# Performance work log

Measured on AMD Instinct MI355X. Metric: run time of the kernel, lower is better.

Reference implementation:

```python
import jax, jax.numpy as jnp
import numpy as np

TOP_K = 2

def setup_inputs() -> dict:
    key = jax.random.key(0)
    k1, k2, k3, k4 = jax.random.split(key, 4)
    T, H, I, E = 8192, 2048, 4096, 8
    s = 0.02
    return {
        "hidden_states": jax.random.normal(k1, (T, H), dtype=jnp.float32),
        "router_w": jax.random.normal(k2, (E, H), dtype=jnp.float32) * s,
        "ws": jax.random.normal(k3, (E, 2 * I, H), dtype=jnp.float32) * s,  # [gate; up]
        "w2s": jax.random.normal(k4, (E, H, I), dtype=jnp.float32) * s,
    }

def reference(hidden_states, router_w, ws, w2s):
    # Router gating: softmax over experts, top-k, NO renormalization
    logits = hidden_states @ router_w.T              # [T, E]
    probs = jax.nn.softmax(logits, axis=-1)
    topv, topi = jax.lax.top_k(probs, TOP_K)         # [T, K]
    T, E = probs.shape
    I = w2s.shape[2]
    # Dense routing-weight matrix [T, E]; top_k indices are unique per token
    w = jnp.zeros_like(probs).at[jnp.arange(T)[:, None], topi].set(topv)
    out = jnp.zeros_like(hidden_states)
    for e in range(E):  # fixed small expert loop; avoids [T,E,2I] blowup
        gate = hidden_states @ ws[e, :I].T           # [T, I]
        up = hidden_states @ ws[e, I:].T             # [T, I]
        h = jax.nn.silu(gate) * up                   # SwiGLU
        out = out + w[:, e:e + 1] * (h @ w2s[e].T)   # combine
    return out
```

## Files before the change

### kernel.cpp

```cpp
#include <hip/hip_runtime.h>
#include <cstdint>
#include <cstddef>

#define T_TOK 8192
#define HDIM  2048
#define IDIM  4096
#define NEXP  8
#define MAXT  72

typedef __bf16 bf16x8 __attribute__((ext_vector_type(8)));
typedef float  f32x4  __attribute__((ext_vector_type(4)));

#define BARRIER() __builtin_amdgcn_s_barrier()
#define VMW(n)    do { asm volatile("s_waitcnt vmcnt(" #n ")" ::: "memory"); } while (0)
#define PRIO1()   __builtin_amdgcn_s_setprio(1)
#define PRIO0()   __builtin_amdgcn_s_setprio(0)

__device__ __forceinline__ unsigned short f2bf(float f) {
    union { float f; unsigned u; } v; v.f = f;
    unsigned r = v.u + 0x7FFFu + ((v.u >> 16) & 1u);
    return (unsigned short)(r >> 16);
}

__device__ __forceinline__ void gload16(const void* g, void* l) {
    __builtin_amdgcn_global_load_lds((__attribute__((address_space(1))) void*)g,
                                     (__attribute__((address_space(3))) void*)l,
                                     16, 0, 0);
}

__global__ __launch_bounds__(256) void router_k(const float* __restrict__ hs,
                                                const float* __restrict__ rw,
                                                float* __restrict__ wgt,
                                                int* __restrict__ counts,
                                                int* __restrict__ lists,
                                                unsigned short* __restrict__ hs_bf) {
    int gid  = blockIdx.x * 256 + threadIdx.x;
    int tok  = gid >> 6;
    int lane = threadIdx.x & 63;
    const float* x = hs + (size_t)tok * HDIM;
    unsigned short* xb = hs_bf + (size_t)tok * HDIM;

    float acc[NEXP];
#pragma unroll
    for (int e = 0; e < NEXP; ++e) acc[e] = 0.f;
    for (int h = lane; h < HDIM; h += 64) {
        float xv = x[h];
        xb[h] = f2bf(xv);
#pragma unroll
        for (int e = 0; e < NEXP; ++e) acc[e] = fmaf(xv, rw[e * HDIM + h], acc[e]);
    }
#pragma unroll
    for (int off = 32; off > 0; off >>= 1) {
#pragma unroll
        for (int e = 0; e < NEXP; ++e) acc[e] += __shfl_xor(acc[e], off, 64);
    }
    if (lane == 0) {
        float m = acc[0];
#pragma unroll
        for (int e = 1; e < NEXP; ++e) m = fmaxf(m, acc[e]);
        float p[NEXP]; float s = 0.f;
#pragma unroll
        for (int e = 0; e < NEXP; ++e) { p[e] = expf(acc[e] - m); s += p[e]; }
        float inv = 1.f / s;
        int i1 = 0;
#pragma unroll
        for (int e = 1; e < NEXP; ++e) if (acc[e] > acc[i1]) i1 = e;
        int i2 = -1;
#pragma unroll
        for (int e = 0; e < NEXP; ++e) if (e != i1 && (i2 < 0 || acc[e] > acc[i2])) i2 = e;
#pragma unroll
        for (int e = 0; e < NEXP; ++e)
            wgt[(size_t)tok * NEXP + e] = (e == i1 || e == i2) ? p[e] * inv : 0.f;
        int p1 = atomicAdd(&counts[i1], 1);
        lists[i1 * T_TOK + p1] = tok;
        int p2 = atomicAdd(&counts[i2], 1);
        lists[i2 * T_TOK + p2] = (1 << 16) | tok;
    }
}

__global__ void plan_k(const int* __restrict__ counts, int* __restrict__ offs,
                       int* __restrict__ desc, int* __restrict__ ntiles) {
    if (threadIdx.x == 0 && blockIdx.x == 0) {
        int off = 0, n = 0;
        for (int e = 0; e < NEXP; ++e) {
            offs[e] = off;
            int nt = (counts[e] + 255) >> 8;
            for (int t = 0; t < nt; ++t) desc[n++] = (e << 16) | t;
            off += nt * 256;
        }
        *ntiles = n;
    }
}

__global__ __launch_bounds__(256) void cvt_k(const float* __restrict__ in,
                                             unsigned short* __restrict__ out, long n4) {
    long i      = (long)blockIdx.x * 256 + threadIdx.x;
    long stride = (long)gridDim.x * 256;
    const float4* in4 = (const float4*)in;
    ushort4* out4 = (ushort4*)out;
    for (long j = i; j < n4; j += stride) {
        float4 v = in4[j];
        ushort4 o;
        o.x = f2bf(v.x); o.y = f2bf(v.y); o.z = f2bf(v.z); o.w = f2bf(v.w);
        out4[j] = o;
    }
}

__global__ __launch_bounds__(512, 2) void gemm1_k(const unsigned short* __restrict__ A,
                                                  const unsigned short* __restrict__ Wall,
                                                  unsigned short* __restrict__ Hout,
                                                  const int* __restrict__ lists,
                                                  const int* __restrict__ counts,
                                                  const int* __restrict__ offs,
                                                  const int* __restrict__ desc,
                                                  const int* __restrict__ ntiles) {
    const int slot = blockIdx.y;
    if (slot >= *ntiles) return;
    const int dsc = desc[slot];
    const int e = dsc >> 16, tt = dsc & 0xFFFF;
    const int cnt = counts[e];
    const int t0 = tt * 256;
    const int* list = lists + e * T_TOK;
    const unsigned short* W = Wall + (size_t)e * 2 * IDIM * HDIM;
    const int hbase = offs[e];
    const int n0 = blockIdx.x * 128;

    extern __shared__ __align__(16) char lds[];

    const int tid  = threadIdx.x;
    const int lane = tid & 63;
    const int wid  = tid >> 6;
    const int wr   = wid >> 2;
    const int wc   = wid & 3;

    const int prow = tid >> 3;
    const int pcol = (tid & 7) * 16;
    const int lcol = (pcol ^ ((prow & 7) << 4)) >> 1;
    unsigned aoff[4];
#pragma unroll
    for (int i = 0; i < 4; ++i) {
        int g = t0 + i * 64 + prow;
        int tok = list[(g < cnt) ? g : t0] & 0xFFFF;
        aoff[i] = (unsigned)tok * HDIM + lcol;
    }
    unsigned goff[2], uoff[2];
#pragma unroll
    for (int i = 0; i < 2; ++i) {
        goff[i] = (unsigned)(n0 + i * 64 + prow) * HDIM + lcol;
        uoff[i] = (unsigned)(IDIM + n0 + i * 64 + prow) * HDIM + lcol;
    }
    const int dst = tid * 16;

#define SG_AH0(b, t) do { unsigned k0_ = (unsigned)((t) & 31) * 64;      \
    gload16(A + aoff[0] + k0_, lds + (b) * 32768 + dst);                 \
    gload16(A + aoff[1] + k0_, lds + (b) * 32768 + 8192 + dst); } while (0)
#define SG_AH1(b, t) do { unsigned k0_ = (unsigned)((t) & 31) * 64;      \
    gload16(A + aoff[2] + k0_, lds + (b) * 32768 + 16384 + dst);         \
    gload16(A + aoff[3] + k0_, lds + (b) * 32768 + 24576 + dst); } while (0)
#define SG_G(b, t) do { unsigned k0_ = (unsigned)((t) & 31) * 64;        \
    gload16(W + goff[0] + k0_, lds + 65536 + (b) * 16384 + dst);         \
    gload16(W + goff[1] + k0_, lds + 65536 + (b) * 16384 + 8192 + dst); } while (0)
#define SG_U(b, t) do { unsigned k0_ = (unsigned)((t) & 31) * 64;        \
    gload16(W + uoff[0] + k0_, lds + 98304 + (b) * 16384 + dst);         \
    gload16(W + uoff[1] + k0_, lds + 98304 + (b) * 16384 + 8192 + dst); } while (0)

    const int frd = (lane & 7) << 4;
    const int cb0 = (((lane >> 4) * 16)     ) ^ frd;
    const int cb1 = (((lane >> 4) * 16) | 64) ^ frd;
    const int arow = (wr * 64 + (lane & 15)) * 128;
    const int brow = (wc * 32 + (lane & 15)) * 128;

    f32x4 accg[8][2], accu[8][2];
#pragma unroll
    for (int mi = 0; mi < 8; ++mi)
#pragma unroll
        for (int ni = 0; ni < 2; ++ni) {
            accg[mi][ni] = (f32x4){0.f, 0.f, 0.f, 0.f};
            accu[mi][ni] = (f32x4){0.f, 0.f, 0.f, 0.f};
        }

    SG_AH0(0, 0); SG_G(0, 0); SG_U(0, 0); SG_AH1(0, 0);
    SG_AH0(1, 1); SG_G(1, 1);
    VMW(4);
    BARRIER();

    const int NT = HDIM / 64;
    for (int kt = 0; kt < NT; ++kt) {
        const int b  = kt & 1;
        const int bn = b ^ 1;
        const char* la = lds + b * 32768 + arow;
        const char* lg = lds + 65536 + b * 16384 + brow;
        const char* lu = lds + 98304 + b * 16384 + brow;
        bf16x8 a0[2][4], bg[2][2], bu[2][2];

#pragma unroll
        for (int mi = 0; mi < 4; ++mi) {
            a0[0][mi] = *(const bf16x8*)(la + mi * 2048 + cb0);
            a0[1][mi] = *(const bf16x8*)(la + mi * 2048 + cb1);
        }
#pragma unroll
        for (int ni = 0; ni < 2; ++ni) {
            bg[0][ni] = *(const bf16x8*)(lg + ni * 2048 + cb0);
            bg[1][ni] = *(const bf16x8*)(lg + ni * 2048 + cb1);
        }
        SG_AH1(bn, kt + 1);
        BARRIER(); PRIO1();
#pragma unroll
        for (int ks = 0; ks < 2; ++ks)
#pragma unroll
            for (int mi = 0; mi < 4; ++mi)
#pragma unroll
                for (int ni = 0; ni < 2; ++ni)
                    accg[mi][ni] = __builtin_amdgcn_mfma_f32_16x16x32_bf16(a0[ks][mi], bg[ks][ni], accg[mi][ni], 0, 0, 0);
        PRIO0(); BARRIER();

#pragma unroll
        for (int ni = 0; ni < 2; ++ni) {
            bu[0][ni] = *(const bf16x8*)(lu + ni * 2048 + cb0);
            bu[1][ni] = *(const bf16x8*)(lu + ni * 2048 + cb1);
        }
        SG_U(bn, kt + 1);
        BARRIER(); PRIO1();
#pragma unroll
        for (int ks = 0; ks < 2; ++ks)
#pragma unroll
            for (int mi = 0; mi < 4; ++mi)
#pragma unroll
                for (int ni = 0; ni < 2; ++ni)
                    accu[mi][ni] = __builtin_amdgcn_mfma_f32_16x16x32_bf16(a0[ks][mi], bu[ks][ni], accu[mi][ni], 0, 0, 0);
        PRIO0(); BARRIER();

#pragma unroll
        for (int mi = 0; mi < 4; ++mi) {
            a0[0][mi] = *(const bf16x8*)(la + 16384 + mi * 2048 + cb0);
            a0[1][mi] = *(const bf16x8*)(la + 16384 + mi * 2048 + cb1);
        }
        SG_AH0(b, kt + 2);
        BARRIER(); PRIO1();
#pragma unroll
        for (int ks = 0; ks < 2; ++ks)
#pragma unroll
            for (int mi = 0; mi < 4; ++mi)
#pragma unroll
                for (int ni = 0; ni < 2; ++ni)
                    accg[mi + 4][ni] = __builtin_amdgcn_mfma_f32_16x16x32_bf16(a0[ks][mi], bg[ks][ni], accg[mi + 4][ni], 0, 0, 0);
        PRIO0(); BARRIER();

        SG_G(b, kt + 2);
        PRIO1();
#pragma unroll
        for (int ks = 0; ks < 2; ++ks)
#pragma unroll
            for (int mi = 0; mi < 4; ++mi)
#pragma unroll
                for (int ni = 0; ni < 2; ++ni)
                    accu[mi + 4][ni] = __builtin_amdgcn_mfma_f32_16x16x32_bf16(a0[ks][mi], bu[ks][ni], accu[mi + 4][ni], 0, 0, 0);
        PRIO0();
        VMW(4);
        BARRIER();
    }
    VMW(0);
#undef SG_AH0
#undef SG_AH1
#undef SG_G
#undef SG_U

#pragma unroll
    for (int mi = 0; mi < 8; ++mi)
#pragma unroll
        for (int ni = 0; ni < 2; ++ni)
#pragma unroll
            for (int j = 0; j < 4; ++j) {
                int qr = mi >> 2, m = mi & 3;
                int row = hbase + t0 + qr * 128 + wr * 64 + m * 16 + ((lane >> 4) << 2) + j;
                int col = n0 + wc * 32 + ni * 16 + (lane & 15);
                float g = accg[mi][ni][j], u = accu[mi][ni][j];
                float hv = (g / (1.f + expf(-g))) * u;
                Hout[(size_t)row * IDIM + col] = f2bf(hv);
            }
}

__global__ __launch_bounds__(512, 2) void gemm2_k(const unsigned short* __restrict__ Ah,
                                                  const unsigned short* __restrict__ Ball,
                                                  const float* __restrict__ wgt,
                                                  float* __restrict__ outP,
                                                  const int* __restrict__ lists,
                                                  const int* __restrict__ counts,
                                                  const int* __restrict__ offs,
                                                  const int* __restrict__ desc,
                                                  const int* __restrict__ ntiles) {
    const int slot = blockIdx.y;
    if (slot >= *ntiles) return;
    const int dsc = desc[slot];
    const int e = dsc >> 16, tt = dsc & 0xFFFF;
    const int cnt = counts[e];
    const int t0 = tt * 256;
    const int* list = lists + e * T_TOK;
    const unsigned short* B = Ball + (size_t)e * HDIM * IDIM;
    const int hbase = offs[e];
    const int n0 = blockIdx.x * 256;

    extern __shared__ __align__(16) char lds[];

    const int tid  = threadIdx.x;
    const int lane = tid & 63;
    const int wid  = tid >> 6;
    const int wr   = wid >> 2;
    const int wc   = wid & 3;

    const int prow = tid >> 3;
    const int pcol = (tid & 7) * 16;
    const int lcol = (pcol ^ ((prow & 7) << 4)) >> 1;
    unsigned aoff[4], boff[4];
#pragma unroll
    for (int i = 0; i < 4; ++i) {
        aoff[i] = (unsigned)(hbase + t0 + i * 64 + prow) * IDIM + lcol;
        boff[i] = (unsigned)(n0 + i * 64 + prow) * IDIM + lcol;
    }
    const int dst = tid * 16;

#define SG_AH0(b, t) do { unsigned k0_ = (unsigned)((t) & 63) * 64;       \
    gload16(Ah + aoff[0] + k0_, lds + (b) * 32768 + dst);                 \
    gload16(Ah + aoff[1] + k0_, lds + (b) * 32768 + 8192 + dst); } while (0)
#define SG_AH1(b, t) do { unsigned k0_ = (unsigned)((t) & 63) * 64;       \
    gload16(Ah + aoff[2] + k0_, lds + (b) * 32768 + 16384 + dst);         \
    gload16(Ah + aoff[3] + k0_, lds + (b) * 32768 + 24576 + dst); } while (0)
#define SG_BH0(b, t) do { unsigned k0_ = (unsigned)((t) & 63) * 64;       \
    gload16(B + boff[0] + k0_, lds + 65536 + (b) * 32768 + dst);          \
    gload16(B + boff[1] + k0_, lds + 65536 + (b) * 32768 + 8192 + dst); } while (0)
#define SG_BH1(b, t) do { unsigned k0_ = (unsigned)((t) & 63) * 64;       \
    gload16(B + boff[2] + k0_, lds + 65536 + (b) * 32768 + 16384 + dst);  \
    gload16(B + boff[3] + k0_, lds + 65536 + (b) * 32768 + 24576 + dst); } while (0)

    const int frd = (lane & 7) << 4;
    const int cb0 = (((lane >> 4) * 16)     ) ^ frd;
    const int cb1 = (((lane >> 4) * 16) | 64) ^ frd;
    const int arow = (wr * 64 + (lane & 15)) * 128;
    const int brow = (wc * 64 + (lane & 15)) * 128;

    f32x4 acc[8][4];
#pragma unroll
    for (int mi = 0; mi < 8; ++mi)
#pragma unroll
        for (int ni = 0; ni < 4; ++ni) acc[mi][ni] = (f32x4){0.f, 0.f, 0.f, 0.f};

    SG_AH0(0, 0); SG_BH0(0, 0); SG_AH1(0, 0); SG_BH1(0, 0);
    SG_AH0(1, 1); SG_BH0(1, 1);
    VMW(0);
    BARRIER();

    const int NT = IDIM / 64;
    for (int kt = 0; kt < NT; ++kt) {
        const int b  = kt & 1;
        const int bn = b ^ 1;
        const char* la = lds + b * 32768 + arow;
        const char* lb = lds + 65536 + b * 32768 + brow;
        bf16x8 a0[2][4], bb[2][4];

#pragma unroll
        for (int mi = 0; mi < 4; ++mi) {
            a0[0][mi] = *(const bf16x8*)(la + mi * 2048 + cb0);
            a0[1][mi] = *(const bf16x8*)(la + mi * 2048 + cb1);
        }
#pragma unroll
        for (int ni = 0; ni < 2; ++ni) {
            bb[0][ni] = *(const bf16x8*)(lb + ni * 2048 + cb0);
            bb[1][ni] = *(const bf16x8*)(lb + ni * 2048 + cb1);
        }
        SG_AH1(bn, kt + 1);
        BARRIER(); PRIO1();
#pragma unroll
        for (int ks = 0; ks < 2; ++ks)
#pragma unroll
            for (int mi = 0; mi < 4; ++mi)
#pragma unroll
                for (int ni = 0; ni < 2; ++ni)
                    acc[mi][ni] = __builtin_amdgcn_mfma_f32_16x16x32_bf16(a0[ks][mi], bb[ks][ni], acc[mi][ni], 0, 0, 0);
        PRIO0(); BARRIER();

#pragma unroll
        for (int ni = 0; ni < 2; ++ni) {
            bb[0][ni + 2] = *(const bf16x8*)(lb + (ni + 2) * 2048 + cb0);
            bb[1][ni + 2] = *(const bf16x8*)(lb + (ni + 2) * 2048 + cb1);
        }
        SG_BH1(bn, kt + 1);
        BARRIER(); PRIO1();
#pragma unroll
        for (int ks = 0; ks < 2; ++ks)
#pragma unroll
            for (int mi = 0; mi < 4; ++mi)
#pragma unroll
                for (int ni = 0; ni < 2; ++ni)
                    acc[mi][ni + 2] = __builtin_amdgcn_mfma_f32_16x16x32_bf16(a0[ks][mi], bb[ks][ni + 2], acc[mi][ni + 2], 0, 0, 0);
        PRIO0(); BARRIER();

#pragma unroll
        for (int mi = 0; mi < 4; ++mi) {
            a0[0][mi] = *(const bf16x8*)(la + 16384 + mi * 2048 + cb0);
            a0[1][mi] = *(const bf16x8*)(la + 16384 + mi * 2048 + cb1);
        }
        SG_AH0(b, kt + 2);
        BARRIER(); PRIO1();
#pragma unroll
        for (int ks = 0; ks < 2; ++ks)
#pragma unroll
            for (int mi = 0; mi < 4; ++mi)
#pragma unroll
                for (int ni = 0; ni < 2; ++ni)
                    acc[mi + 4][ni] = __builtin_amdgcn_mfma_f32_16x16x32_bf16(a0[ks][mi], bb[ks][ni], acc[mi + 4][ni], 0, 0, 0);
        PRIO0(); BARRIER();

        SG_BH0(b, kt + 2);
        PRIO1();
#pragma unroll
        for (int ks = 0; ks < 2; ++ks)
#pragma unroll
            for (int mi = 0; mi < 4; ++mi)
#pragma unroll
                for (int ni = 0; ni < 2; ++ni)
                    acc[mi + 4][ni + 2] = __builtin_amdgcn_mfma_f32_16x16x32_bf16(a0[ks][mi], bb[ks][ni + 2], acc[mi + 4][ni + 2], 0, 0, 0);
        PRIO0();
        VMW(4);
        BARRIER();
    }
    VMW(0);
#undef SG_AH0
#undef SG_AH1
#undef SG_BH0
#undef SG_BH1

#pragma unroll
    for (int mi = 0; mi < 8; ++mi) {
        int qr = mi >> 2, m = mi & 3;
#pragma unroll
        for (int j = 0; j < 4; ++j) {
            int g = t0 + qr * 128 + wr * 64 + m * 16 + ((lane >> 4) << 2) + j;
            if (g < cnt) {
                int ent = list[g];
                int tok = ent & 0xFFFF;
                int sl  = ent >> 16;
                float w = wgt[(size_t)tok * NEXP + e];
                float* o = outP + (size_t)sl * T_TOK * HDIM + (size_t)tok * HDIM;
#pragma unroll
                for (int ni = 0; ni < 4; ++ni) {
                    int col = n0 + wc * 64 + ni * 16 + (lane & 15);
                    o[col] = w * acc[mi][ni][j];
                }
            }
        }
    }
}

__global__ __launch_bounds__(256) void combine_k(const float* __restrict__ p0,
                                                 const float* __restrict__ p1,
                                                 float* __restrict__ out, long n4) {
    long i      = (long)blockIdx.x * 256 + threadIdx.x;
    long stride = (long)gridDim.x * 256;
    const float4* a4 = (const float4*)p0;
    const float4* b4 = (const float4*)p1;
    float4* o4 = (float4*)out;
    for (long j = i; j < n4; j += stride) {
        float4 a = a4[j], b = b4[j];
        o4[j] = make_float4(a.x + b.x, a.y + b.y, a.z + b.z, a.w + b.w);
    }
}

extern "C" void kernel_launch(void* const* d_in, const int* in_sizes, int n_in,
                              void* d_out, int out_size, void* d_ws, size_t ws_size,
                              hipStream_t stream) {
    const float* hs  = (const float*)d_in[0];
    const float* rw  = (const float*)d_in[1];
    const float* ws  = (const float*)d_in[2];
    const float* w2s = (const float*)d_in[3];
    float* out = (float*)d_out;

    char* wsp = (char*)d_ws;
    unsigned short* hs_bf = (unsigned short*)(wsp);
    unsigned short* w_bf  = (unsigned short*)(wsp + 33554432ULL);
    unsigned short* w2_bf = (unsigned short*)(wsp + 301989888ULL);
    unsigned short* h_bf  = (unsigned short*)(wsp + 436207616ULL);
    float*          outP  = (float*)(wsp + 587202560ULL);
    float*          wgt   = (float*)(wsp + 721420288ULL);
    int*            counts = (int*)(wsp + 721682432ULL);
    int*            offs   = (int*)(wsp + 721682560ULL);
    int*            lists  = (int*)(wsp + 721682688ULL);
    int*            desc   = (int*)(wsp + 721944832ULL);
    int*            ntiles = (int*)(wsp + 721945344ULL);

    hipMemsetAsync(counts, 0, NEXP * sizeof(int), stream);
    cvt_k<<<4096, 256, 0, stream>>>(ws, w_bf, (long)NEXP * 2 * IDIM * HDIM / 4);
    cvt_k<<<4096, 256, 0, stream>>>(w2s, w2_bf, (long)NEXP * HDIM * IDIM / 4);
    router_k<<<(T_TOK * 64) / 256, 256, 0, stream>>>(hs, rw, wgt, counts, lists, hs_bf);
    plan_k<<<1, 64, 0, stream>>>(counts, offs, desc, ntiles);

    gemm1_k<<<dim3(IDIM / 128, MAXT), 512, 131072, stream>>>(
        hs_bf, w_bf, h_bf, lists, counts, offs, desc, ntiles);
    gemm2_k<<<dim3(HDIM / 256, MAXT), 512, 131072, stream>>>(
        h_bf, w2_bf, wgt, outP, lists, counts, offs, desc, ntiles);
    combine_k<<<2048, 256, 0, stream>>>(outP, outP + (size_t)T_TOK * HDIM, out,
                                        (long)T_TOK * HDIM / 4);
}
```

Baseline: 1.368 ms.

## Software-pipeline LDS fragment reads across iterations and drop redundant barriers

Both MoE GEMM kernels now load the next k-tile's A and B fragments from LDS at the end of the current iteration, so each phase's LDS reads overlap the MFMAs of the phase before. Separate a1 and b23 register sets let fragment loads run ahead of the matching compute. This removes several barriers per iteration and moves the vmcnt wait ahead of the prefetch reads. The down-projection prologue now waits with vmcnt(4) instead of 0. The cost is higher register pressure and a tighter ordering argument between LDS reads and async global-to-LDS writes into the other buffer.

```diff
diff --git a/kernel.cpp b/kernel.cpp
--- a/kernel.cpp
+++ b/kernel.cpp
@@ -184,27 +184,38 @@
     VMW(4);
     BARRIER();
 
+    bf16x8 a0[2][4], a1[2][4], bg[2][2], bu[2][2];
+    {
+        const char* la = lds + arow;
+        const char* lg = lds + 65536 + brow;
+#pragma unroll
+        for (int mi = 0; mi < 4; ++mi) {
+            a0[0][mi] = *(const bf16x8*)(la + mi * 2048 + cb0);
+            a0[1][mi] = *(const bf16x8*)(la + mi * 2048 + cb1);
+        }
+#pragma unroll
+        for (int ni = 0; ni < 2; ++ni) {
+            bg[0][ni] = *(const bf16x8*)(lg + ni * 2048 + cb0);
+            bg[1][ni] = *(const bf16x8*)(lg + ni * 2048 + cb1);
+        }
+    }
+
     const int NT = HDIM / 64;
     for (int kt = 0; kt < NT; ++kt) {
         const int b  = kt & 1;
         const int bn = b ^ 1;
-        const char* la = lds + b * 32768 + arow;
-        const char* lg = lds + 65536 + b * 16384 + brow;
-        const char* lu = lds + 98304 + b * 16384 + brow;
-        bf16x8 a0[2][4], bg[2][2], bu[2][2];
-
-#pragma unroll
-        for (int mi = 0; mi < 4; ++mi) {
-            a0[0][mi] = *(const bf16x8*)(la + mi * 2048 + cb0);
-            a0[1][mi] = *(const bf16x8*)(la + mi * 2048 + cb1);
-        }
-#pragma unroll
-        for (int ni = 0; ni < 2; ++ni) {
-            bg[0][ni] = *(const bf16x8*)(lg + ni * 2048 + cb0);
-            bg[1][ni] = *(const bf16x8*)(lg + ni * 2048 + cb1);
+        const char* la  = lds + b * 32768 + arow;
+        const char* lu  = lds + 98304 + b * 16384 + brow;
+        const char* lan = lds + bn * 32768 + arow;
+        const char* lgn = lds + 65536 + bn * 16384 + brow;
+
+#pragma unroll
+        for (int ni = 0; ni < 2; ++ni) {
+            bu[0][ni] = *(const bf16x8*)(lu + ni * 2048 + cb0);
+            bu[1][ni] = *(const bf16x8*)(lu + ni * 2048 + cb1);
         }
         SG_AH1(bn, kt + 1);
-        BARRIER(); PRIO1();
+        PRIO1();
 #pragma unroll
         for (int ks = 0; ks < 2; ++ks)
 #pragma unroll
@@ -215,12 +226,12 @@
         PRIO0(); BARRIER();
 
 #pragma unroll
-        for (int ni = 0; ni < 2; ++ni) {
-            bu[0][ni] = *(const bf16x8*)(lu + ni * 2048 + cb0);
-            bu[1][ni] = *(const bf16x8*)(lu + ni * 2048 + cb1);
+        for (int mi = 0; mi < 4; ++mi) {
+            a1[0][mi] = *(const bf16x8*)(la + 16384 + mi * 2048 + cb0);
+            a1[1][mi] = *(const bf16x8*)(la + 16384 + mi * 2048 + cb1);
         }
         SG_U(bn, kt + 1);
-        BARRIER(); PRIO1();
+        PRIO1();
 #pragma unroll
         for (int ks = 0; ks < 2; ++ks)
 #pragma unroll
@@ -230,33 +241,39 @@
                     accu[mi][ni] = __builtin_amdgcn_mfma_f32_16x16x32_bf16(a0[ks][mi], bu[ks][ni], accu[mi][ni], 0, 0, 0);
         PRIO0(); BARRIER();
 
+        SG_AH0(b, kt + 2);
+        PRIO1();
+#pragma unroll
+        for (int ks = 0; ks < 2; ++ks)
+#pragma unroll
+            for (int mi = 0; mi < 4; ++mi)
+#pragma unroll
+                for (int ni = 0; ni < 2; ++ni)
+                    accg[mi + 4][ni] = __builtin_amdgcn_mfma_f32_16x16x32_bf16(a1[ks][mi], bg[ks][ni], accg[mi + 4][ni], 0, 0, 0);
+        PRIO0(); BARRIER();
+
+        SG_G(b, kt + 2);
+        VMW(4);
+        BARRIER();
 #pragma unroll
         for (int mi = 0; mi < 4; ++mi) {
-            a0[0][mi] = *(const bf16x8*)(la + 16384 + mi * 2048 + cb0);
-            a0[1][mi] = *(const bf16x8*)(la + 16384 + mi * 2048 + cb1);
-        }
-        SG_AH0(b, kt + 2);
-        BARRIER(); PRIO1();
-#pragma unroll
-        for (int ks = 0; ks < 2; ++ks)
-#pragma unroll
-            for (int mi = 0; mi < 4; ++mi)
-#pragma unroll
-                for (int ni = 0; ni < 2; ++ni)
-                    accg[mi + 4][ni] = __builtin_amdgcn_mfma_f32_16x16x32_bf16(a0[ks][mi], bg[ks][ni], accg[mi + 4][ni], 0, 0, 0);
-        PRIO0(); BARRIER();
-
-        SG_G(b, kt + 2);
-        PRIO1();
-#pragma unroll
-        for (int ks = 0; ks < 2; ++ks)
-#pragma unroll
-            for (int mi = 0; mi < 4; ++mi)
-#pragma unroll
-                for (int ni = 0; ni < 2; ++ni)
-                    accu[mi + 4][ni] = __builtin_amdgcn_mfma_f32_16x16x32_bf16(a0[ks][mi], bu[ks][ni], accu[mi + 4][ni], 0, 0, 0);
+            a0[0][mi] = *(const bf16x8*)(lan + mi * 2048 + cb0);
+            a0[1][mi] = *(const bf16x8*)(lan + mi * 2048 + cb1);
+        }
+#pragma unroll
+        for (int ni = 0; ni < 2; ++ni) {
+            bg[0][ni] = *(const bf16x8*)(lgn + ni * 2048 + cb0);
+            bg[1][ni] = *(const bf16x8*)(lgn + ni * 2048 + cb1);
+        }
+        PRIO1();
+#pragma unroll
+        for (int ks = 0; ks < 2; ++ks)
+#pragma unroll
+            for (int mi = 0; mi < 4; ++mi)
+#pragma unroll
+                for (int ni = 0; ni < 2; ++ni)
+                    accu[mi + 4][ni] = __builtin_amdgcn_mfma_f32_16x16x32_bf16(a1[ks][mi], bu[ks][ni], accu[mi + 4][ni], 0, 0, 0);
         PRIO0();
-        VMW(4);
         BARRIER();
     }
     VMW(0);
@@ -346,81 +363,99 @@
 
     SG_AH0(0, 0); SG_BH0(0, 0); SG_AH1(0, 0); SG_BH1(0, 0);
     SG_AH0(1, 1); SG_BH0(1, 1);
-    VMW(0);
+    VMW(4);
     BARRIER();
+
+    bf16x8 a0[2][4], a1[2][4], b01[2][2], b23[2][2];
+    {
+        const char* la = lds + arow;
+        const char* lb = lds + 65536 + brow;
+#pragma unroll
+        for (int mi = 0; mi < 4; ++mi) {
+            a0[0][mi] = *(const bf16x8*)(la + mi * 2048 + cb0);
+            a0[1][mi] = *(const bf16x8*)(la + mi * 2048 + cb1);
+        }
+#pragma unroll
+        for (int ni = 0; ni < 2; ++ni) {
+            b01[0][ni] = *(const bf16x8*)(lb + ni * 2048 + cb0);
+            b01[1][ni] = *(const bf16x8*)(lb + ni * 2048 + cb1);
+        }
+    }
 
     const int NT = IDIM / 64;
     for (int kt = 0; kt < NT; ++kt) {
         const int b  = kt & 1;
         const int bn = b ^ 1;
-        const char* la = lds + b * 32768 + arow;
-        const char* lb = lds + 65536 + b * 32768 + brow;
-        bf16x8 a0[2][4], bb[2][4];
+        const char* la  = lds + b * 32768 + arow;
+        const char* lb  = lds + 65536 + b * 32768 + brow;
+        const char* lan = lds + bn * 32768 + arow;
+        const char* lbn = lds + 65536 + bn * 32768 + brow;
+
+#pragma unroll
+        for (int ni = 0; ni < 2; ++ni) {
+            b23[0][ni] = *(const bf16x8*)(lb + (ni + 2) * 2048 + cb0);
+            b23[1][ni] = *(const bf16x8*)(lb + (ni + 2) * 2048 + cb1);
+        }
+        SG_AH1(bn, kt + 1);
+        PRIO1();
+#pragma unroll
+        for (int ks = 0; ks < 2; ++ks)
+#pragma unroll
+            for (int mi = 0; mi < 4; ++mi)
+#pragma unroll
+                for (int ni = 0; ni < 2; ++ni)
+                    acc[mi][ni] = __builtin_amdgcn_mfma_f32_16x16x32_bf16(a0[ks][mi], b01[ks][ni], acc[mi][ni], 0, 0, 0);
+        PRIO0(); BARRIER();
 
 #pragma unroll
         for (int mi = 0; mi < 4; ++mi) {
-            a0[0][mi] = *(const bf16x8*)(la + mi * 2048 + cb0);
-            a0[1][mi] = *(const bf16x8*)(la + mi * 2048 + cb1);
-        }
-#pragma unroll
-        for (int ni = 0; ni < 2; ++ni) {
-            bb[0][ni] = *(const bf16x8*)(lb + ni * 2048 + cb0);
-            bb[1][ni] = *(const bf16x8*)(lb + ni * 2048 + cb1);
-        }
-        SG_AH1(bn, kt + 1);
-        BARRIER(); PRIO1();
-#pragma unroll
-        for (int ks = 0; ks < 2; ++ks)
-#pragma unroll
-            for (int mi = 0; mi < 4; ++mi)
-#pragma unroll
-                for (int ni = 0; ni < 2; ++ni)
-                    acc[mi][ni] = __builtin_amdgcn_mfma_f32_16x16x32_bf16(a0[ks][mi], bb[ks][ni], acc[mi][ni], 0, 0, 0);
+            a1[0][mi] = *(const bf16x8*)(la + 16384 + mi * 2048 + cb0);
+            a1[1][mi] = *(const bf16x8*)(la + 16384 + mi * 2048 + cb1);
+        }
+        SG_BH1(bn, kt + 1);
+        PRIO1();
+#pragma unroll
+        for (int ks = 0; ks < 2; ++ks)
+#pragma unroll
+            for (int mi = 0; mi < 4; ++mi)
+#pragma unroll
+                for (int ni = 0; ni < 2; ++ni)
+                    acc[mi][ni + 2] = __builtin_amdgcn_mfma_f32_16x16x32_bf16(a0[ks][mi], b23[ks][ni], acc[mi][ni + 2], 0, 0, 0);
         PRIO0(); BARRIER();
 
-#pragma unroll
-        for (int ni = 0; ni < 2; ++ni) {
-            bb[0][ni + 2] = *(const bf16x8*)(lb + (ni + 2) * 2048 + cb0);
-            bb[1][ni + 2] = *(const bf16x8*)(lb + (ni + 2) * 2048 + cb1);
-        }
-        SG_BH1(bn, kt + 1);
-        BARRIER(); PRIO1();
-#pragma unroll
-        for (int ks = 0; ks < 2; ++ks)
-#pragma unroll
-            for (int mi = 0; mi < 4; ++mi)
-#pragma unroll
-                for (int ni = 0; ni < 2; ++ni)
-                    acc[mi][ni + 2] = __builtin_amdgcn_mfma_f32_16x16x32_bf16(a0[ks][mi], bb[ks][ni + 2], acc[mi][ni + 2], 0, 0, 0);
+        SG_AH0(b, kt + 2);
+        PRIO1();
+#pragma unroll
+        for (int ks = 0; ks < 2; ++ks)
+#pragma unroll
+            for (int mi = 0; mi < 4; ++mi)
+#pragma unroll
+                for (int ni = 0; ni < 2; ++ni)
+                    acc[mi + 4][ni] = __builtin_amdgcn_mfma_f32_16x16x32_bf16(a1[ks][mi], b01[ks][ni], acc[mi + 4][ni], 0, 0, 0);
         PRIO0(); BARRIER();
 
+        SG_BH0(b, kt + 2);
+        VMW(4);
+        BARRIER();
 #pragma unroll
         for (int mi = 0; mi < 4; ++mi) {
-            a0[0][mi] = *(const bf16x8*)(la + 16384 + mi * 2048 + cb0);
-            a0[1][mi] = *(const bf16x8*)(la + 16384 + mi * 2048 + cb1);
-        }
-        SG_AH0(b, kt + 2);
-        BARRIER(); PRIO1();
-#pragma unroll
-        for (int ks = 0; ks < 2; ++ks)
-#pragma unroll
-            for (int mi = 0; mi < 4; ++mi)
-#pragma unroll
-                for (int ni = 0; ni < 2; ++ni)
-                    acc[mi + 4][ni] = __builtin_amdgcn_mfma_f32_16x16x32_bf16(a0[ks][mi], bb[ks][ni], acc[mi + 4][ni], 0, 0, 0);
-        PRIO0(); BARRIER();
-
-        SG_BH0(b, kt + 2);
-        PRIO1();
-#pragma unroll
-        for (int ks = 0; ks < 2; ++ks)
-#pragma unroll
-            for (int mi = 0; mi < 4; ++mi)
-#pragma unroll
-                for (int ni = 0; ni < 2; ++ni)
-                    acc[mi + 4][ni + 2] = __builtin_amdgcn_mfma_f32_16x16x32_bf16(a0[ks][mi], bb[ks][ni + 2], acc[mi + 4][ni + 2], 0, 0, 0);
+            a0[0][mi] = *(const bf16x8*)(lan + mi * 2048 + cb0);
+            a0[1][mi] = *(const bf16x8*)(lan + mi * 2048 + cb1);
+        }
+#pragma unroll
+        for (int ni = 0; ni < 2; ++ni) {
+            b01[0][ni] = *(const bf16x8*)(lbn + ni * 2048 + cb0);
+            b01[1][ni] = *(const bf16x8*)(lbn + ni * 2048 + cb1);
+        }
+        PRIO1();
+#pragma unroll
+        for (int ks = 0; ks < 2; ++ks)
+#pragma unroll
+            for (int mi = 0; mi < 4; ++mi)
+#pragma unroll
+                for (int ni = 0; ni < 2; ++ni)
+                    acc[mi + 4][ni + 2] = __builtin_amdgcn_mfma_f32_16x16x32_bf16(a1[ks][mi], b23[ks][ni], acc[mi + 4][ni + 2], 0, 0, 0);
         PRIO0();
-        VMW(4);
         BARRIER();
     }
     VMW(0);
```

After: 1.349 ms, median of 3. Within noise of the previous version (-1.4%).
